# Performance work log

Measured on AMD Instinct MI355X. Metric: run time of the kernel, lower is better.

The kernel has to match this reference:

```python
import jax, jax.numpy as jnp
import numpy as np
import math

DIM = 256
B, S = 4, 2048


def setup_inputs() -> dict:
    key = jax.random.key(0)
    ks = jax.random.split(key, 8)
    h = DIM // 2
    return {
        "features": jax.random.normal(ks[0], (B, S, DIM), dtype=jnp.float32),
        "W1": jax.random.normal(ks[1], (DIM, h), dtype=jnp.float32) / np.sqrt(DIM),
        "b1": jnp.zeros((h,), dtype=jnp.float32),
        "ln_g": jnp.ones((h,), dtype=jnp.float32),
        "ln_b": jnp.zeros((h,), dtype=jnp.float32),
        "W2": jax.random.normal(ks[2], (h, 1), dtype=jnp.float32) / np.sqrt(h),
        "b2": jnp.zeros((1,), dtype=jnp.float32),
        "target_entropy": jnp.full((1,), math.log(DIM), dtype=jnp.float32),
        "temperature": jnp.ones((1,), dtype=jnp.float32),
    }


def _compute_entropy(features, temperature):
    b, s, d = features.shape
    x = features.reshape(-1, d)  # [N, D]
    sq = jnp.sum(x * x, axis=-1)  # [N]
    # squared euclidean distance (cdist(...)**2), clamped for numerical safety
    d2 = jnp.maximum(sq[:, None] + sq[None, :] - 2.0 * (x @ x.T), 0.0)  # [N, N]
    kernel = jnp.exp(-d2 / (2.0 * temperature[0] ** 2))
    probs = kernel / jnp.sum(kernel, axis=-1, keepdims=True)
    entropy = -jnp.sum(probs * jnp.log(probs + 1e-6), axis=-1)
    return entropy.reshape(b, s)


def _entropy_estimator(features, W1, b1, ln_g, ln_b, W2, b2):
    h = features @ W1 + b1  # [B, S, D/2]
    mu = jnp.mean(h, axis=-1, keepdims=True)
    var = jnp.mean((h - mu) ** 2, axis=-1, keepdims=True)
    hn = (h - mu) / jnp.sqrt(var + 1e-5) * ln_g + ln_b
    hg = jax.nn.gelu(hn, approximate=False)
    return (hg @ W2 + b2).squeeze(-1)  # [B, S]


def reference(features, W1, b1, ln_g, ln_b, W2, b2, target_entropy, temperature):
    current_entropy = _compute_entropy(features, temperature)  # [B, S]
    # estimated_entropy is computed in the original forward but unused in outputs
    _est = _entropy_estimator(features, W1, b1, ln_g, ln_b, W2, b2)
    entropy_diff = current_entropy - target_entropy[0]
    control_signal = jax.nn.sigmoid(-entropy_diff / temperature[0])  # [B, S]
    controlled_features = features * control_signal[..., None]
    return controlled_features, control_signal
```

## Files before the change

kernel.cpp:

```cpp
#include <hip/hip_runtime.h>

#define N 8192
#define D 256

typedef short short8 __attribute__((ext_vector_type(8)));
typedef float f32x4 __attribute__((ext_vector_type(4)));

__device__ __forceinline__ unsigned short f2bf(float f) {
    unsigned int u = __float_as_uint(f);
    u += 0x7fffu + ((u >> 16) & 1u);
    return (unsigned short)(u >> 16);
}
__device__ __forceinline__ float bf2f(unsigned short h) {
    return __uint_as_float(((unsigned int)h) << 16);
}

__global__ __launch_bounds__(64) void k_cvt(const float* __restrict__ x,
                                            unsigned short* __restrict__ xb2,
                                            float* __restrict__ sq,
                                            float* __restrict__ Sarr,
                                            float* __restrict__ Larr) {
    const int lane = threadIdx.x & 63;
    const int c = lane & 15, q8 = lane >> 4;
    const int grp = blockIdx.x;
    const int row = grp * 16 + c;

    float ssum = 0.0f;
#pragma unroll
    for (int kk = 0; kk < 8; ++kk) {
        const float4* gp = (const float4*)(x + (size_t)row * D + kk * 32 + q8 * 8);
        float4 v0 = gp[0], v1 = gp[1];
        unsigned short h[8];
        h[0] = f2bf(v0.x); h[1] = f2bf(v0.y); h[2] = f2bf(v0.z); h[3] = f2bf(v0.w);
        h[4] = f2bf(v1.x); h[5] = f2bf(v1.y); h[6] = f2bf(v1.z); h[7] = f2bf(v1.w);
        short8 p;
#pragma unroll
        for (int i = 0; i < 8; ++i) {
            float f = bf2f(h[i]);
            ssum = fmaf(f, f, ssum);
            p[i] = (short)h[i];
        }
        ((short8*)xb2)[(grp * 8 + kk) * 64 + lane] = p;
    }
    ssum += __shfl_xor(ssum, 16, 64);
    ssum += __shfl_xor(ssum, 32, 64);
    if (q8 == 0) {
        sq[row] = ssum;
        Sarr[row] = 0.0f;
        Larr[row] = 0.0f;
    }
}

__device__ __forceinline__ void ld_b(const short8* __restrict__ xb8, int grp,
                                     int lane, short8 (&bv)[8]) {
#pragma unroll
    for (int kk = 0; kk < 8; ++kk)
        bv[kk] = xb8[(size_t)grp * 512 + kk * 64 + lane];
}

__device__ __forceinline__ void ct_compute(const short8 (&av)[4][8],
                                           const short8 (&bv)[8],
                                           float bc, const float (&ar)[16],
                                           float armax, float c2,
                                           float (&Sr)[16], float (&Mr)[16]) {
    f32x4 acc[4];
#pragma unroll
    for (int tr = 0; tr < 4; ++tr)
#pragma unroll
        for (int r = 0; r < 4; ++r) acc[tr][r] = 0.0f;

#pragma unroll
    for (int kk = 0; kk < 8; ++kk)
#pragma unroll
        for (int tr = 0; tr < 4; ++tr)
            acc[tr] = __builtin_amdgcn_mfma_f32_16x16x32_bf16(
                av[tr][kk], bv[kk], acc[tr], 0, 0, 0);

    float gmax = acc[0][0];
#pragma unroll
    for (int tr = 0; tr < 4; ++tr)
#pragma unroll
        for (int r = 0; r < 4; ++r) gmax = fmaxf(gmax, acc[tr][r]);
    const float bound = fmaf(gmax, c2, armax + bc);

    if (__any(bound >= -115.0f)) {
#pragma unroll
        for (int tr = 0; tr < 4; ++tr)
#pragma unroll
            for (int r = 0; r < 4; ++r) {
                float g = acc[tr][r];
                float t2 = fminf(fmaf(g, c2, ar[tr * 4 + r] + bc), 0.0f);
                float e = __builtin_amdgcn_exp2f(t2);
                Sr[tr * 4 + r] += e;
                Mr[tr * 4 + r] = fmaf(e, t2, Mr[tr * 4 + r]);
            }
    }
}

__global__ __launch_bounds__(256, 2) void k_gram(const unsigned short* __restrict__ xb2,
                                                 const float* __restrict__ sq,
                                                 const float* __restrict__ temp,
                                                 float* __restrict__ Sarr,
                                                 float* __restrict__ Larr) {
    const int tid = threadIdx.x;
    const int wv = tid >> 6, lane = tid & 63;
    const int q8 = lane >> 4, c = lane & 15;
    const int rowbase = blockIdx.x * 256;
    const int ybase = blockIdx.y * 512;
    const float T = temp[0];
    const float LOG2E = 1.44269504f;
    const float s2 = -LOG2E / (2.0f * T * T);
    const float c2 = -2.0f * s2;

    short8 av[4][8];
#pragma unroll
    for (int tr = 0; tr < 4; ++tr) {
        const int grp = (rowbase >> 4) + wv * 4 + tr;
#pragma unroll
        for (int kk = 0; kk < 8; ++kk)
            av[tr][kk] = ((const short8*)xb2)[(grp * 8 + kk) * 64 + lane];
    }
    float ar[16];
#pragma unroll
    for (int tr = 0; tr < 4; ++tr)
#pragma unroll
        for (int r = 0; r < 4; ++r)
            ar[tr * 4 + r] = sq[rowbase + wv * 64 + tr * 16 + q8 * 4 + r] * s2;
    float armax = ar[0];
#pragma unroll
    for (int k = 1; k < 16; ++k) armax = fmaxf(armax, ar[k]);

    float Sr[16], Mr[16];
#pragma unroll
    for (int k = 0; k < 16; ++k) { Sr[k] = 0.f; Mr[k] = 0.f; }

    const short8* xb8 = (const short8*)xb2;
    const int gbase = ybase >> 4;

    short8 bvA[8], bvB[8];
    float bcA, bcB;
    ld_b(xb8, gbase, lane, bvA);
    bcA = sq[ybase + c] * s2;

    for (int ct = 0; ct < 32; ct += 2) {
        ld_b(xb8, gbase + ct + 1, lane, bvB);
        bcB = sq[ybase + (ct + 1) * 16 + c] * s2;

        ct_compute(av, bvA, bcA, ar, armax, c2, Sr, Mr);

        const int nx = (ct + 2 < 32) ? ct + 2 : 0;
        ld_b(xb8, gbase + nx, lane, bvA);
        bcA = sq[ybase + nx * 16 + c] * s2;

        ct_compute(av, bvB, bcB, ar, armax, c2, Sr, Mr);
    }

#pragma unroll
    for (int m = 1; m <= 8; m <<= 1)
#pragma unroll
        for (int k = 0; k < 16; ++k) {
            Sr[k] += __shfl_xor(Sr[k], m, 64);
            Mr[k] += __shfl_xor(Mr[k], m, 64);
        }
    if (c == 0) {
        const float LN2 = 0.69314718f;
#pragma unroll
        for (int k = 0; k < 16; ++k) {
            int row = rowbase + wv * 64 + (k >> 2) * 16 + q8 * 4 + (k & 3);
            atomicAdd(&Sarr[row], Sr[k]);
            atomicAdd(&Larr[row], Mr[k] * LN2);
        }
    }
}

__global__ __launch_bounds__(256) void k_finish(const float* __restrict__ x,
                                                const float* __restrict__ Sarr,
                                                const float* __restrict__ Larr,
                                                const float* __restrict__ target,
                                                const float* __restrict__ temp,
                                                float* __restrict__ out) {
    const int gid = blockIdx.x * 256 + threadIdx.x;
    const int row = gid >> 6;
    float S = Sarr[row], L = Larr[row];
    float H = __logf(S) - L / S;
    float z = (H - target[0]) / temp[0];
    float cs = 1.0f / (1.0f + __expf(z));
    float4 v = ((const float4*)x)[gid];
    float4 o;
    o.x = v.x * cs; o.y = v.y * cs; o.z = v.z * cs; o.w = v.w * cs;
    ((float4*)out)[gid] = o;
    if ((gid & 63) == 0) out[(size_t)N * D + row] = cs;
}

extern "C" void kernel_launch(void* const* d_in, const int* in_sizes, int n_in,
                              void* d_out, int out_size, void* d_ws, size_t ws_size,
                              hipStream_t stream) {
    const float* x = (const float*)d_in[0];
    const float* target = (const float*)d_in[7];
    const float* temp = (const float*)d_in[8];
    float* out = (float*)d_out;

    float* wsf = (float*)d_ws;
    float* sq = wsf;
    float* Sarr = wsf + N;
    float* Larr = wsf + 2 * N;

    const size_t need = 3 * (size_t)N * sizeof(float) + (size_t)N * D * sizeof(unsigned short);
    unsigned short* xb2 = (ws_size >= need) ? (unsigned short*)(wsf + 3 * N)
                                            : (unsigned short*)d_out;

    k_cvt<<<N / 16, 64, 0, stream>>>(x, xb2, sq, Sarr, Larr);
    k_gram<<<dim3(32, 16), 256, 0, stream>>>(xb2, sq, temp, Sarr, Larr);
    k_finish<<<(N * (D / 4)) / 256, 256, 0, stream>>>(x, Sarr, Larr, target, temp, out);
}
```

Baseline: 108.2 us.

## Fuse convert, gram and finish kernels into one cooperative launch

Merges the three kernel launches into a single cooperative kernel of 512 blocks, using grid-wide syncs between the bf16 conversion, the Gram/entropy accumulation and the final scaling phases. This is meant to remove launch gaps and inter-kernel drain/fill overhead. It requires all 512 blocks to be co-resident (2 per CU), and grid sync has its own cost. If the cooperative launch fails, the code falls back to the original three launches.

```diff
diff --git a/kernel.cpp b/kernel.cpp
--- a/kernel.cpp
+++ b/kernel.cpp
@@ -1,4 +1,7 @@
 #include <hip/hip_runtime.h>
+#include <hip/hip_cooperative_groups.h>
+
+namespace cg = cooperative_groups;
 
 #define N 8192
 #define D 256
@@ -15,14 +18,60 @@
     return __uint_as_float(((unsigned int)h) << 16);
 }
 
-__global__ __launch_bounds__(64) void k_cvt(const float* __restrict__ x,
-                                            unsigned short* __restrict__ xb2,
-                                            float* __restrict__ sq,
-                                            float* __restrict__ Sarr,
-                                            float* __restrict__ Larr) {
-    const int lane = threadIdx.x & 63;
+__device__ __forceinline__ void ld_b(const short8* __restrict__ xb8, int grp,
+                                     int lane, short8 (&bv)[8]) {
+#pragma unroll
+    for (int kk = 0; kk < 8; ++kk)
+        bv[kk] = xb8[(size_t)grp * 512 + kk * 64 + lane];
+}
+
+__device__ __forceinline__ void ct_compute(const short8 (&av)[4][8],
+                                           const short8 (&bv)[8],
+                                           float bc, const float (&ar)[16],
+                                           float armax, float c2,
+                                           float (&Sr)[16], float (&Mr)[16]) {
+    f32x4 acc[4];
+#pragma unroll
+    for (int tr = 0; tr < 4; ++tr)
+#pragma unroll
+        for (int r = 0; r < 4; ++r) acc[tr][r] = 0.0f;
+
+#pragma unroll
+    for (int kk = 0; kk < 8; ++kk)
+#pragma unroll
+        for (int tr = 0; tr < 4; ++tr)
+            acc[tr] = __builtin_amdgcn_mfma_f32_16x16x32_bf16(
+                av[tr][kk], bv[kk], acc[tr], 0, 0, 0);
+
+    float gmax = acc[0][0];
+#pragma unroll
+    for (int tr = 0; tr < 4; ++tr)
+#pragma unroll
+        for (int r = 0; r < 4; ++r) gmax = fmaxf(gmax, acc[tr][r]);
+    const float bound = fmaf(gmax, c2, armax + bc);
+
+    if (__any(bound >= -115.0f)) {
+#pragma unroll
+        for (int tr = 0; tr < 4; ++tr)
+#pragma unroll
+            for (int r = 0; r < 4; ++r) {
+                float g = acc[tr][r];
+                float t2 = fminf(fmaf(g, c2, ar[tr * 4 + r] + bc), 0.0f);
+                float e = __builtin_amdgcn_exp2f(t2);
+                Sr[tr * 4 + r] += e;
+                Mr[tr * 4 + r] = fmaf(e, t2, Mr[tr * 4 + r]);
+            }
+    }
+}
+
+
+__device__ __forceinline__ void cvt_body(const float* __restrict__ x,
+                                         unsigned short* __restrict__ xb2,
+                                         float* __restrict__ sq,
+                                         float* __restrict__ Sarr,
+                                         float* __restrict__ Larr,
+                                         int grp, int lane) {
     const int c = lane & 15, q8 = lane >> 4;
-    const int grp = blockIdx.x;
     const int row = grp * 16 + c;
 
     float ssum = 0.0f;
@@ -51,66 +100,16 @@
     }
 }
 
-__device__ __forceinline__ void ld_b(const short8* __restrict__ xb8, int grp,
-                                     int lane, short8 (&bv)[8]) {
-#pragma unroll
-    for (int kk = 0; kk < 8; ++kk)
-        bv[kk] = xb8[(size_t)grp * 512 + kk * 64 + lane];
-}
-
-__device__ __forceinline__ void ct_compute(const short8 (&av)[4][8],
-                                           const short8 (&bv)[8],
-                                           float bc, const float (&ar)[16],
-                                           float armax, float c2,
-                                           float (&Sr)[16], float (&Mr)[16]) {
-    f32x4 acc[4];
-#pragma unroll
-    for (int tr = 0; tr < 4; ++tr)
-#pragma unroll
-        for (int r = 0; r < 4; ++r) acc[tr][r] = 0.0f;
-
-#pragma unroll
-    for (int kk = 0; kk < 8; ++kk)
-#pragma unroll
-        for (int tr = 0; tr < 4; ++tr)
-            acc[tr] = __builtin_amdgcn_mfma_f32_16x16x32_bf16(
-                av[tr][kk], bv[kk], acc[tr], 0, 0, 0);
-
-    float gmax = acc[0][0];
-#pragma unroll
-    for (int tr = 0; tr < 4; ++tr)
-#pragma unroll
-        for (int r = 0; r < 4; ++r) gmax = fmaxf(gmax, acc[tr][r]);
-    const float bound = fmaf(gmax, c2, armax + bc);
-
-    if (__any(bound >= -115.0f)) {
-#pragma unroll
-        for (int tr = 0; tr < 4; ++tr)
-#pragma unroll
-            for (int r = 0; r < 4; ++r) {
-                float g = acc[tr][r];
-                float t2 = fminf(fmaf(g, c2, ar[tr * 4 + r] + bc), 0.0f);
-                float e = __builtin_amdgcn_exp2f(t2);
-                Sr[tr * 4 + r] += e;
-                Mr[tr * 4 + r] = fmaf(e, t2, Mr[tr * 4 + r]);
-            }
-    }
-}
-
-__global__ __launch_bounds__(256, 2) void k_gram(const unsigned short* __restrict__ xb2,
-                                                 const float* __restrict__ sq,
-                                                 const float* __restrict__ temp,
-                                                 float* __restrict__ Sarr,
-                                                 float* __restrict__ Larr) {
-    const int tid = threadIdx.x;
+__device__ __forceinline__ void gram_body(const unsigned short* __restrict__ xb2,
+                                          const float* __restrict__ sq,
+                                          float s2, float c2,
+                                          float* __restrict__ Sarr,
+                                          float* __restrict__ Larr,
+                                          int bx, int by, int tid) {
     const int wv = tid >> 6, lane = tid & 63;
     const int q8 = lane >> 4, c = lane & 15;
-    const int rowbase = blockIdx.x * 256;
-    const int ybase = blockIdx.y * 512;
-    const float T = temp[0];
-    const float LOG2E = 1.44269504f;
-    const float s2 = -LOG2E / (2.0f * T * T);
-    const float c2 = -2.0f * s2;
+    const int rowbase = bx * 256;
+    const int ybase = by * 512;
 
     short8 av[4][8];
 #pragma unroll
@@ -173,13 +172,12 @@
     }
 }
 
-__global__ __launch_bounds__(256) void k_finish(const float* __restrict__ x,
-                                                const float* __restrict__ Sarr,
-                                                const float* __restrict__ Larr,
-                                                const float* __restrict__ target,
-                                                const float* __restrict__ temp,
-                                                float* __restrict__ out) {
-    const int gid = blockIdx.x * 256 + threadIdx.x;
+__device__ __forceinline__ void finish_body(const float* __restrict__ x,
+                                            const float* __restrict__ Sarr,
+                                            const float* __restrict__ Larr,
+                                            const float* __restrict__ target,
+                                            const float* __restrict__ temp,
+                                            float* __restrict__ out, int gid) {
     const int row = gid >> 6;
     float S = Sarr[row], L = Larr[row];
     float H = __logf(S) - L / S;
@@ -192,6 +190,69 @@
     if ((gid & 63) == 0) out[(size_t)N * D + row] = cs;
 }
 
+__global__ __launch_bounds__(256, 2) void k_fused(const float* __restrict__ x,
+                                                  unsigned short* __restrict__ xb2,
+                                                  float* __restrict__ sq,
+                                                  float* __restrict__ Sarr,
+                                                  float* __restrict__ Larr,
+                                                  const float* __restrict__ target,
+                                                  const float* __restrict__ temp,
+                                                  float* __restrict__ out) {
+    const int bid = blockIdx.x;
+    const int tid = threadIdx.x;
+    const int wv = tid >> 6, lane = tid & 63;
+
+    if (bid < 128) cvt_body(x, xb2, sq, Sarr, Larr, bid * 4 + wv, lane);
+
+    cg::this_grid().sync();
+
+    {
+        const float T = temp[0];
+        const float LOG2E = 1.44269504f;
+        const float s2 = -LOG2E / (2.0f * T * T);
+        const float c2 = -2.0f * s2;
+        gram_body(xb2, sq, s2, c2, Sarr, Larr, bid & 31, bid >> 5, tid);
+    }
+
+    cg::this_grid().sync();
+
+    {
+        const int stride = 512 * 256;
+        for (int gid = bid * 256 + tid; gid < N * (D / 4); gid += stride)
+            finish_body(x, Sarr, Larr, target, temp, out, gid);
+    }
+}
+
+
+__global__ __launch_bounds__(64) void k_cvt(const float* __restrict__ x,
+                                            unsigned short* __restrict__ xb2,
+                                            float* __restrict__ sq,
+                                            float* __restrict__ Sarr,
+                                            float* __restrict__ Larr) {
+    cvt_body(x, xb2, sq, Sarr, Larr, blockIdx.x, threadIdx.x & 63);
+}
+
+__global__ __launch_bounds__(256, 2) void k_gram(const unsigned short* __restrict__ xb2,
+                                                 const float* __restrict__ sq,
+                                                 const float* __restrict__ temp,
+                                                 float* __restrict__ Sarr,
+                                                 float* __restrict__ Larr) {
+    const float T = temp[0];
+    const float LOG2E = 1.44269504f;
+    const float s2 = -LOG2E / (2.0f * T * T);
+    const float c2 = -2.0f * s2;
+    gram_body(xb2, sq, s2, c2, Sarr, Larr, blockIdx.x, blockIdx.y, threadIdx.x);
+}
+
+__global__ __launch_bounds__(256) void k_finish(const float* __restrict__ x,
+                                                const float* __restrict__ Sarr,
+                                                const float* __restrict__ Larr,
+                                                const float* __restrict__ target,
+                                                const float* __restrict__ temp,
+                                                float* __restrict__ out) {
+    finish_body(x, Sarr, Larr, target, temp, out, blockIdx.x * 256 + threadIdx.x);
+}
+
 extern "C" void kernel_launch(void* const* d_in, const int* in_sizes, int n_in,
                               void* d_out, int out_size, void* d_ws, size_t ws_size,
                               hipStream_t stream) {
@@ -209,7 +270,14 @@
     unsigned short* xb2 = (ws_size >= need) ? (unsigned short*)(wsf + 3 * N)
                                             : (unsigned short*)d_out;
 
-    k_cvt<<<N / 16, 64, 0, stream>>>(x, xb2, sq, Sarr, Larr);
-    k_gram<<<dim3(32, 16), 256, 0, stream>>>(xb2, sq, temp, Sarr, Larr);
-    k_finish<<<(N * (D / 4)) / 256, 256, 0, stream>>>(x, Sarr, Larr, target, temp, out);
-}
+    void* args[] = {(void*)&x, (void*)&xb2, (void*)&sq, (void*)&Sarr,
+                    (void*)&Larr, (void*)&target, (void*)&temp, (void*)&out};
+    hipError_t err = hipLaunchCooperativeKernel((const void*)k_fused,
+                                                dim3(512), dim3(256),
+                                                args, 0, stream);
+    if (err != hipSuccess) {
+        k_cvt<<<N / 16, 64, 0, stream>>>(x, xb2, sq, Sarr, Larr);
+        k_gram<<<dim3(32, 16), 256, 0, stream>>>(xb2, sq, temp, Sarr, Larr);
+        k_finish<<<(N * (D / 4)) / 256, 256, 0, stream>>>(x, Sarr, Larr, target, temp, out);
+    }
+}
```

New measurement: 247.7 us. 129% more time.
